# Kernel tuning notes

Hardware: AMD Instinct MI355X
Metric: run time of the kernel (lower is better)

Reference implementation:

```python
import jax, jax.numpy as jnp
import numpy as np

C, N, B = 16, 65536, 4096  # cases, points per case, batch of case IDs


def _w(key, fan_in, fan_out):
    return jax.random.normal(key, (fan_in, fan_out), dtype=jnp.float32) / np.sqrt(fan_in).astype(np.float32)


def setup_inputs() -> dict:
    key = jax.random.key(0)
    ks = jax.random.split(key, 8)
    pts = jax.random.normal(ks[0], (C, N, 3), dtype=jnp.float32)
    inp = {
        "pts": pts,
        "W1_0": _w(ks[1], 3, 64), "b1_0": jnp.zeros((64,), jnp.float32),
        "W1_1": _w(ks[2], 64, 128), "b1_1": jnp.zeros((128,), jnp.float32),
        "W1_2": _w(ks[3], 128, 512), "b1_2": jnp.zeros((512,), jnp.float32),
        "W2_0": _w(ks[4], 512, 256), "b2_0": jnp.zeros((256,), jnp.float32),
        "W2_1": _w(ks[5], 256, 512), "b2_1": jnp.zeros((512,), jnp.float32),
        "x": jax.random.randint(ks[6], (B,), 0, C, dtype=jnp.int64),
    }
    return inp


def reference(pts, W1_0, b1_0, W1_1, b1_1, W1_2, b1_2, W2_0, b2_0, W2_1, b2_1, x):
    def mlp1(h):  # shared per-point MLP, SiLU after every layer
        h = jax.nn.silu(h @ W1_0 + b1_0)
        h = jax.nn.silu(h @ W1_1 + b1_1)
        h = jax.nn.silu(h @ W1_2 + b1_2)
        return h

    feats = mlp1(pts)                       # [C, N, F1]
    idx = jnp.argmax(feats, axis=1)         # [C, F1] critical-point indices per feature
    # gather critical points (detached in the torch original)
    fixed = jax.lax.stop_gradient(pts[jnp.arange(pts.shape[0])[:, None], idx])  # [C, F1, 3]

    feats2 = mlp1(fixed)                    # [C, F1, F1]
    latent0 = jnp.max(feats2, axis=1)       # [C, F1]

    h = jax.nn.silu(latent0 @ W2_0 + b2_0)  # [C, 256]
    latent = h @ W2_1 + b2_1                # [C, total_modes*ge_features]

    caseID_unit = jax.nn.one_hot(x, latent.shape[0], dtype=latent.dtype)  # [B, C]
    return caseID_unit @ latent             # [B, 512]
```

## Files before the change

### kernel.cpp

```cpp
#include <hip/hip_runtime.h>
#include <math.h>

#define NCASES   16
#define NPTS_BIG 65536
#define F1       512
#define OUT_B    4096

typedef __attribute__((ext_vector_type(8))) short  short8;
typedef __attribute__((ext_vector_type(4))) float  floatx4;

__device__ __forceinline__ float silu_f(float x) {
    return x * __builtin_amdgcn_rcpf(1.0f + __expf(-x));
}

__device__ __forceinline__ unsigned f2bf_hi(float x) {
    unsigned u = __float_as_uint(x);
    return u + 0x7FFFu + ((u >> 16) & 1u);
}
__device__ __forceinline__ unsigned short f2bf(float x) {
    return (unsigned short)(f2bf_hi(x) >> 16);
}
__device__ __forceinline__ unsigned pk2bf_rtz(float lo, float hi) {
    return __builtin_amdgcn_perm(__float_as_uint(hi), __float_as_uint(lo), 0x07060302u);
}

__device__ __forceinline__ unsigned enc_f(float x) {
    unsigned u = __float_as_uint(x);
    return (u & 0x80000000u) ? ~u : (u | 0x80000000u);
}
__device__ __forceinline__ float dec_f(unsigned e) {
    unsigned u = (e & 0x80000000u) ? (e ^ 0x80000000u) : ~e;
    return __uint_as_float(u);
}

__device__ __forceinline__ float sgpr_f(float x) {
    return __uint_as_float(__builtin_amdgcn_readfirstlane(__float_as_uint(x)));
}

__global__ void k_prep(const float* __restrict__ W11, const float* __restrict__ W12,
                       unsigned short* __restrict__ BbWs, unsigned short* __restrict__ BcWs,
                       unsigned long long* __restrict__ argBufs)
{
    int i = blockIdx.x * 256 + threadIdx.x;
    if (i < 16384) argBufs[i] = 0ull;
    {
        int j = i & 7, l = (i >> 3) & 63, t = i >> 9;
        int KT = t & 3, NT = (t >> 2) & 3, w = t >> 4;
        int k = KT * 32 + (l >> 4) * 8 + j;
        int f = w * 64 + NT * 16 + (l & 15);
        BcWs[i] = f2bf(W12[(size_t)k * 512 + f]);
    }
    if (i < 8192) {
        int j = i & 7, l = (i >> 3) & 63, t = i >> 9;
        int KT = t & 1, w = t >> 1;
        int k = KT * 32 + (l >> 4) * 8 + j;
        int f = w * 16 + (l & 15);
        BbWs[i] = f2bf(W11[(size_t)k * 128 + f]);
    }
}

template<bool GATHER>
__global__ __launch_bounds__(512, 4)
void k_mlp1_argmax(const float* __restrict__ pts, int nPts, int chunksPerBlock,
                   const unsigned long long* __restrict__ gatherIdx,
                   const float* __restrict__ W10, const float* __restrict__ b10,
                   const float* __restrict__ b11, const float* __restrict__ b12,
                   const unsigned short* __restrict__ BbWs,
                   const unsigned short* __restrict__ BcWs,
                   unsigned long long* __restrict__ argOut)
{
    const int c   = blockIdx.y;
    const int tid = threadIdx.x;
    const int w   = tid >> 6;
    const int l   = tid & 63;
    const int lm  = l & 15;
    const int q   = l >> 4;

    __shared__ __align__(16) unsigned short s_h0[2][64][72];
    __shared__ __align__(16) unsigned short s_h1[2][64][136];

    const int wf = __builtin_amdgcn_readfirstlane(w);

    float wA0[8], wA1[8], wA2[8], bA[8];
    #pragma unroll
    for (int j = 0; j < 8; ++j) {
        wA0[j] = sgpr_f(W10[  0 + wf * 8 + j]);
        wA1[j] = sgpr_f(W10[ 64 + wf * 8 + j]);
        wA2[j] = sgpr_f(W10[128 + wf * 8 + j]);
        bA[j]  = sgpr_f(b10[       wf * 8 + j]);
    }

    short8 Bc[16];
    #pragma unroll
    for (int t = 0; t < 16; ++t)
        Bc[t] = *(const short8*)(BcWs + (size_t)((wf * 16 + t) * 64 + l) * 8);
    short8 Bb[2];
    #pragma unroll
    for (int t = 0; t < 2; ++t)
        Bb[t] = *(const short8*)(BbWs + (size_t)((wf * 2 + t) * 64 + l) * 8);

    const float bias11 = b11[wf * 16 + lm];
    const floatx4 bias4 = {bias11, bias11, bias11, bias11};
    const floatx4 zero4 = {0.f, 0.f, 0.f, 0.f};

    float bestv[4];
    #pragma unroll
    for (int NT = 0; NT < 4; ++NT) bestv[NT] = -INFINITY;

    const float* cpts = pts + (size_t)c * nPts * 3;

    auto ldpt = [&](int ch, float& x, float& y, float& z) {
        const int pbase = (blockIdx.x * chunksPerBlock + ch) * 64;
        if (GATHER) {
            unsigned gi = ~(unsigned)(gatherIdx[(size_t)c * 512 + pbase + l] & 0xFFFFFFFFull);
            const float* sp = cpts + (size_t)gi * 3;
            x = sp[0]; y = sp[1]; z = sp[2];
        } else {
            const float* sp = cpts + (size_t)(pbase + l) * 3;
            x = sp[0]; y = sp[1]; z = sp[2];
        }
    };
    auto stageA = [&](int p, float x, float y, float z) {
        float v[8];
        #pragma unroll
        for (int j = 0; j < 8; ++j) {
            float t = fmaf(z, wA2[j], bA[j]);
            t = fmaf(y, wA1[j], t);
            t = fmaf(x, wA0[j], t);
            v[j] = silu_f(t);
        }
        uint4 hv = { pk2bf_rtz(v[0], v[1]), pk2bf_rtz(v[2], v[3]),
                     pk2bf_rtz(v[4], v[5]), pk2bf_rtz(v[6], v[7]) };
        *(uint4*)&s_h0[p][l][wf * 8] = hv;
    };

    {
        float x, y, z;
        ldpt(0, x, y, z);
        stageA(0, x, y, z);
    }
    __syncthreads();

    for (int ch = 0; ch < chunksPerBlock; ++ch) {
        const int p = ch & 1;
        const bool more = (ch + 1 < chunksPerBlock);

        float nx, ny, nz;
        if (more) ldpt(ch + 1, nx, ny, nz);

        #pragma unroll
        for (int MT = 0; MT < 4; ++MT) {
            short8 a0 = *(const short8*)&s_h0[p][MT * 16 + lm][q * 8];
            short8 a1 = *(const short8*)&s_h0[p][MT * 16 + lm][32 + q * 8];
            floatx4 acc = __builtin_amdgcn_mfma_f32_16x16x32_bf16(a0, Bb[0], bias4, 0, 0, 0);
            acc = __builtin_amdgcn_mfma_f32_16x16x32_bf16(a1, Bb[1], acc, 0, 0, 0);
            #pragma unroll
            for (int r = 0; r < 4; ++r) {
                unsigned uv = __float_as_uint(silu_f(acc[r]));
                s_h1[p][MT * 16 + q * 4 + r][wf * 16 + lm] = (unsigned short)(uv >> 16);
            }
        }

        if (more) stageA(p ^ 1, nx, ny, nz);

        __syncthreads();

        const int cb0 = 127 - (ch << 4);
        #pragma unroll
        for (int MT = 0; MT < 4; ++MT) {
            short8 a[4];
            #pragma unroll
            for (int KT = 0; KT < 4; ++KT)
                a[KT] = *(const short8*)&s_h1[p][MT * 16 + lm][KT * 32 + q * 8];
            const int cbM = cb0 - (MT << 2);
            #pragma unroll
            for (int NT = 0; NT < 4; ++NT) {
                floatx4 acc = __builtin_amdgcn_mfma_f32_16x16x32_bf16(a[0], Bc[NT * 4 + 0], zero4, 0, 0, 0);
                #pragma unroll
                for (int KT = 1; KT < 4; ++KT)
                    acc = __builtin_amdgcn_mfma_f32_16x16x32_bf16(a[KT], Bc[NT * 4 + KT], acc, 0, 0, 0);
                float x0 = __uint_as_float((__float_as_uint(acc[0]) & 0xFFFFFF80u) | (unsigned)(cbM));
                float x1 = __uint_as_float((__float_as_uint(acc[1]) & 0xFFFFFF80u) | (unsigned)(cbM - 1));
                float x2 = __uint_as_float((__float_as_uint(acc[2]) & 0xFFFFFF80u) | (unsigned)(cbM - 2));
                float x3 = __uint_as_float((__float_as_uint(acc[3]) & 0xFFFFFF80u) | (unsigned)(cbM - 3));
                float t0 = fmaxf(fmaxf(x0, x1), x2);
                bestv[NT] = fmaxf(fmaxf(t0, x3), bestv[NT]);
            }
        }
    }

    #pragma unroll
    for (int NT = 0; NT < 4; ++NT) {
        unsigned u = __float_as_uint(bestv[NT]);
        int t = 127 - (int)(u & 127u);
        unsigned idx = (unsigned)((blockIdx.x * chunksPerBlock + (t >> 4)) * 64
                                  + ((t >> 2) & 3) * 16 + q * 4 + (t & 3));
        float v = __uint_as_float(u & 0xFFFFFF80u) + b12[wf * 64 + NT * 16 + lm];
        #pragma unroll
        for (int m = 16; m <= 32; m <<= 1) {
            float    vo = __shfl_xor(v, m, 64);
            unsigned io = __shfl_xor(idx, m, 64);
            if (vo > v || (vo == v && io < idx)) { v = vo; idx = io; }
        }
        if (q == 0) {
            unsigned long long key = ((unsigned long long)enc_f(v) << 32)
                                   | (unsigned long long)(~idx);
            atomicMax(&argOut[(size_t)c * 512 + wf * 64 + NT * 16 + lm], key);
        }
    }
}

__global__ __launch_bounds__(256)
void k_head(const unsigned long long* __restrict__ argBuf2,
            const float* __restrict__ W20, const float* __restrict__ b20,
            const float* __restrict__ W21, const float* __restrict__ b21,
            float* __restrict__ latent)
{
    const int c = blockIdx.x, tid = threadIdx.x;
    __shared__ float l0[512];
    __shared__ float hh[256];
    l0[tid]       = silu_f(dec_f((unsigned)(argBuf2[(size_t)c * 512 + tid] >> 32)));
    l0[tid + 256] = silu_f(dec_f((unsigned)(argBuf2[(size_t)c * 512 + tid + 256] >> 32)));
    __syncthreads();
    float acc = b20[tid];
    for (int k = 0; k < 512; ++k) acc += l0[k] * W20[(size_t)k * 256 + tid];
    hh[tid] = silu_f(acc);
    __syncthreads();
    #pragma unroll
    for (int r = 0; r < 2; ++r) {
        int f = tid + r * 256;
        float a2 = b21[f];
        for (int k = 0; k < 256; ++k) a2 += hh[k] * W21[(size_t)k * 512 + f];
        latent[(size_t)c * 512 + f] = a2;
    }
}

__global__ void k_scatter(const int* __restrict__ x,
                          const float* __restrict__ latent,
                          float* __restrict__ out)
{
    const int b = blockIdx.x, t = threadIdx.x;
    int cid = x[b];
    const float4* src = (const float4*)(latent + (size_t)cid * 512);
    float4* dst = (float4*)(out + (size_t)b * 512);
    dst[t] = src[t];
}

extern "C" void kernel_launch(void* const* d_in, const int* in_sizes, int n_in,
                              void* d_out, int out_size, void* d_ws, size_t ws_size,
                              hipStream_t stream)
{
    const float* pts = (const float*)d_in[0];
    const float* W10 = (const float*)d_in[1];
    const float* b10 = (const float*)d_in[2];
    const float* W11 = (const float*)d_in[3];
    const float* b11 = (const float*)d_in[4];
    const float* W12 = (const float*)d_in[5];
    const float* b12 = (const float*)d_in[6];
    const float* W20 = (const float*)d_in[7];
    const float* b20 = (const float*)d_in[8];
    const float* W21 = (const float*)d_in[9];
    const float* b21 = (const float*)d_in[10];
    const int*   x   = (const int*)d_in[11];
    float* out = (float*)d_out;

    char* ws = (char*)d_ws;
    unsigned long long* argBuf  = (unsigned long long*)ws;
    unsigned long long* argBuf2 = (unsigned long long*)(ws + 65536);
    float* latent               = (float*)(ws + 131072);
    unsigned short* BbWs        = (unsigned short*)(ws + 163840);
    unsigned short* BcWs        = (unsigned short*)(ws + 180224);

    k_prep<<<dim3(256), dim3(256), 0, stream>>>(W11, W12, BbWs, BcWs, argBuf);

    k_mlp1_argmax<false><<<dim3(128, NCASES), dim3(512), 0, stream>>>(
        pts, NPTS_BIG, 8, nullptr, W10, b10, b11, b12, BbWs, BcWs, argBuf);

    k_mlp1_argmax<true><<<dim3(8, NCASES), dim3(512), 0, stream>>>(
        pts, NPTS_BIG, 1, argBuf, W10, b10, b11, b12, BbWs, BcWs, argBuf2);

    k_head<<<dim3(NCASES), dim3(256), 0, stream>>>(argBuf2, W20, b20, W21, b21, latent);

    k_scatter<<<dim3(OUT_B), dim3(128), 0, stream>>>(x, latent, out);
}
```

Measured before the change: 263.1 us.

## Fuse gathered second MLP pass and head MLP into one per-case tail kernel

Replaces the gather-mode argmax kernel (8x16 blocks with 64-bit atomics into a second buffer) and the separate head kernel with a single k_tail kernel, one 512-thread block per case. Each block runs the per-point MLP over the 512 gathered critical points, tracks only the max (no index), then applies the two head layers from shared memory. This removes one launch, the second argmax buffer, its zeroing and the atomics. In exchange the gathered pass runs on only 16 blocks instead of 128, so it has less parallelism.

Result: slower. 272.3 us (+3.5%).

```diff
diff --git a/kernel.cpp b/kernel.cpp
--- a/kernel.cpp
+++ b/kernel.cpp
@@ -8,6 +8,7 @@
 
 typedef __attribute__((ext_vector_type(8))) short  short8;
 typedef __attribute__((ext_vector_type(4))) float  floatx4;
+typedef unsigned short ush;
 
 __device__ __forceinline__ float silu_f(float x) {
     return x * __builtin_amdgcn_rcpf(1.0f + __expf(-x));
@@ -17,8 +18,8 @@
     unsigned u = __float_as_uint(x);
     return u + 0x7FFFu + ((u >> 16) & 1u);
 }
-__device__ __forceinline__ unsigned short f2bf(float x) {
-    return (unsigned short)(f2bf_hi(x) >> 16);
+__device__ __forceinline__ ush f2bf(float x) {
+    return (ush)(f2bf_hi(x) >> 16);
 }
 __device__ __forceinline__ unsigned pk2bf_rtz(float lo, float hi) {
     return __builtin_amdgcn_perm(__float_as_uint(hi), __float_as_uint(lo), 0x07060302u);
@@ -28,21 +29,16 @@
     unsigned u = __float_as_uint(x);
     return (u & 0x80000000u) ? ~u : (u | 0x80000000u);
 }
-__device__ __forceinline__ float dec_f(unsigned e) {
-    unsigned u = (e & 0x80000000u) ? (e ^ 0x80000000u) : ~e;
-    return __uint_as_float(u);
-}
 
 __device__ __forceinline__ float sgpr_f(float x) {
     return __uint_as_float(__builtin_amdgcn_readfirstlane(__float_as_uint(x)));
 }
 
 __global__ void k_prep(const float* __restrict__ W11, const float* __restrict__ W12,
-                       unsigned short* __restrict__ BbWs, unsigned short* __restrict__ BcWs,
-                       unsigned long long* __restrict__ argBufs)
+                       ush* __restrict__ BbWs, ush* __restrict__ BcWs,
+                       unsigned long long* __restrict__ argBuf)
 {
     int i = blockIdx.x * 256 + threadIdx.x;
-    if (i < 16384) argBufs[i] = 0ull;
     {
         int j = i & 7, l = (i >> 3) & 63, t = i >> 9;
         int KT = t & 3, NT = (t >> 2) & 3, w = t >> 4;
@@ -51,6 +47,7 @@
         BcWs[i] = f2bf(W12[(size_t)k * 512 + f]);
     }
     if (i < 8192) {
+        argBuf[i] = 0ull;
         int j = i & 7, l = (i >> 3) & 63, t = i >> 9;
         int KT = t & 1, w = t >> 1;
         int k = KT * 32 + (l >> 4) * 8 + j;
@@ -59,14 +56,12 @@
     }
 }
 
-template<bool GATHER>
 __global__ __launch_bounds__(512, 4)
 void k_mlp1_argmax(const float* __restrict__ pts, int nPts, int chunksPerBlock,
-                   const unsigned long long* __restrict__ gatherIdx,
                    const float* __restrict__ W10, const float* __restrict__ b10,
                    const float* __restrict__ b11, const float* __restrict__ b12,
-                   const unsigned short* __restrict__ BbWs,
-                   const unsigned short* __restrict__ BcWs,
+                   const ush* __restrict__ BbWs,
+                   const ush* __restrict__ BcWs,
                    unsigned long long* __restrict__ argOut)
 {
     const int c   = blockIdx.y;
@@ -76,8 +71,8 @@
     const int lm  = l & 15;
     const int q   = l >> 4;
 
-    __shared__ __align__(16) unsigned short s_h0[2][64][72];
-    __shared__ __align__(16) unsigned short s_h1[2][64][136];
+    __shared__ __align__(16) ush s_h0[2][64][72];
+    __shared__ __align__(16) ush s_h1[2][64][136];
 
     const int wf = __builtin_amdgcn_readfirstlane(w);
 
@@ -111,14 +106,8 @@
 
     auto ldpt = [&](int ch, float& x, float& y, float& z) {
         const int pbase = (blockIdx.x * chunksPerBlock + ch) * 64;
-        if (GATHER) {
-            unsigned gi = ~(unsigned)(gatherIdx[(size_t)c * 512 + pbase + l] & 0xFFFFFFFFull);
-            const float* sp = cpts + (size_t)gi * 3;
-            x = sp[0]; y = sp[1]; z = sp[2];
-        } else {
-            const float* sp = cpts + (size_t)(pbase + l) * 3;
-            x = sp[0]; y = sp[1]; z = sp[2];
-        }
+        const float* sp = cpts + (size_t)(pbase + l) * 3;
+        x = sp[0]; y = sp[1]; z = sp[2];
     };
     auto stageA = [&](int p, float x, float y, float z) {
         float v[8];
@@ -157,7 +146,7 @@
             #pragma unroll
             for (int r = 0; r < 4; ++r) {
                 unsigned uv = __float_as_uint(silu_f(acc[r]));
-                s_h1[p][MT * 16 + q * 4 + r][wf * 16 + lm] = (unsigned short)(uv >> 16);
+                s_h1[p][MT * 16 + q * 4 + r][wf * 16 + lm] = (ush)(uv >> 16);
             }
         }
 
@@ -210,28 +199,155 @@
     }
 }
 
-__global__ __launch_bounds__(256)
-void k_head(const unsigned long long* __restrict__ argBuf2,
+__global__ __launch_bounds__(512, 4)
+void k_tail(const float* __restrict__ pts, int nPts,
+            const unsigned long long* __restrict__ argBuf,
+            const float* __restrict__ W10, const float* __restrict__ b10,
+            const float* __restrict__ b11, const float* __restrict__ b12,
+            const ush* __restrict__ BbWs,
+            const ush* __restrict__ BcWs,
             const float* __restrict__ W20, const float* __restrict__ b20,
             const float* __restrict__ W21, const float* __restrict__ b21,
             float* __restrict__ latent)
 {
-    const int c = blockIdx.x, tid = threadIdx.x;
-    __shared__ float l0[512];
-    __shared__ float hh[256];
-    l0[tid]       = silu_f(dec_f((unsigned)(argBuf2[(size_t)c * 512 + tid] >> 32)));
-    l0[tid + 256] = silu_f(dec_f((unsigned)(argBuf2[(size_t)c * 512 + tid + 256] >> 32)));
+    const int c   = blockIdx.x;
+    const int tid = threadIdx.x;
+    const int w   = tid >> 6;
+    const int l   = tid & 63;
+    const int lm  = l & 15;
+    const int q   = l >> 4;
+
+    __shared__ __align__(16) ush s_h0[2][64][72];
+    __shared__ __align__(16) ush s_h1[2][64][136];
+    __shared__ float s_l0[512];
+    __shared__ float s_hh[256];
+
+    const int wf = __builtin_amdgcn_readfirstlane(w);
+
+    float wA0[8], wA1[8], wA2[8], bA[8];
+    #pragma unroll
+    for (int j = 0; j < 8; ++j) {
+        wA0[j] = sgpr_f(W10[  0 + wf * 8 + j]);
+        wA1[j] = sgpr_f(W10[ 64 + wf * 8 + j]);
+        wA2[j] = sgpr_f(W10[128 + wf * 8 + j]);
+        bA[j]  = sgpr_f(b10[       wf * 8 + j]);
+    }
+
+    short8 Bc[16];
+    #pragma unroll
+    for (int t = 0; t < 16; ++t)
+        Bc[t] = *(const short8*)(BcWs + (size_t)((wf * 16 + t) * 64 + l) * 8);
+    short8 Bb[2];
+    #pragma unroll
+    for (int t = 0; t < 2; ++t)
+        Bb[t] = *(const short8*)(BbWs + (size_t)((wf * 2 + t) * 64 + l) * 8);
+
+    const float bias11 = b11[wf * 16 + lm];
+    const floatx4 bias4 = {bias11, bias11, bias11, bias11};
+    const floatx4 zero4 = {0.f, 0.f, 0.f, 0.f};
+
+    float bestv[4];
+    #pragma unroll
+    for (int NT = 0; NT < 4; ++NT) bestv[NT] = -INFINITY;
+
+    const float* cpts = pts + (size_t)c * nPts * 3;
+
+    auto ldpt = [&](int ch, float& x, float& y, float& z) {
+        unsigned gi = ~(unsigned)(argBuf[(size_t)c * 512 + ch * 64 + l] & 0xFFFFFFFFull);
+        const float* sp = cpts + (size_t)gi * 3;
+        x = sp[0]; y = sp[1]; z = sp[2];
+    };
+    auto stageA = [&](int p, float x, float y, float z) {
+        float v[8];
+        #pragma unroll
+        for (int j = 0; j < 8; ++j) {
+            float t = fmaf(z, wA2[j], bA[j]);
+            t = fmaf(y, wA1[j], t);
+            t = fmaf(x, wA0[j], t);
+            v[j] = silu_f(t);
+        }
+        uint4 hv = { pk2bf_rtz(v[0], v[1]), pk2bf_rtz(v[2], v[3]),
+                     pk2bf_rtz(v[4], v[5]), pk2bf_rtz(v[6], v[7]) };
+        *(uint4*)&s_h0[p][l][wf * 8] = hv;
+    };
+
+    {
+        float x, y, z;
+        ldpt(0, x, y, z);
+        stageA(0, x, y, z);
+    }
     __syncthreads();
-    float acc = b20[tid];
-    for (int k = 0; k < 512; ++k) acc += l0[k] * W20[(size_t)k * 256 + tid];
-    hh[tid] = silu_f(acc);
+
+    #pragma unroll 1
+    for (int ch = 0; ch < 8; ++ch) {
+        const int p = ch & 1;
+        const bool more = (ch + 1 < 8);
+
+        float nx, ny, nz;
+        if (more) ldpt(ch + 1, nx, ny, nz);
+
+        #pragma unroll
+        for (int MT = 0; MT < 4; ++MT) {
+            short8 a0 = *(const short8*)&s_h0[p][MT * 16 + lm][q * 8];
+            short8 a1 = *(const short8*)&s_h0[p][MT * 16 + lm][32 + q * 8];
+            floatx4 acc = __builtin_amdgcn_mfma_f32_16x16x32_bf16(a0, Bb[0], bias4, 0, 0, 0);
+            acc = __builtin_amdgcn_mfma_f32_16x16x32_bf16(a1, Bb[1], acc, 0, 0, 0);
+            #pragma unroll
+            for (int r = 0; r < 4; ++r) {
+                unsigned uv = __float_as_uint(silu_f(acc[r]));
+                s_h1[p][MT * 16 + q * 4 + r][wf * 16 + lm] = (ush)(uv >> 16);
+            }
+        }
+
+        if (more) stageA(p ^ 1, nx, ny, nz);
+
+        __syncthreads();
+
+        #pragma unroll
+        for (int MT = 0; MT < 4; ++MT) {
+            short8 a[4];
+            #pragma unroll
+            for (int KT = 0; KT < 4; ++KT)
+                a[KT] = *(const short8*)&s_h1[p][MT * 16 + lm][KT * 32 + q * 8];
+            #pragma unroll
+            for (int NT = 0; NT < 4; ++NT) {
+                floatx4 acc = __builtin_amdgcn_mfma_f32_16x16x32_bf16(a[0], Bc[NT * 4 + 0], zero4, 0, 0, 0);
+                #pragma unroll
+                for (int KT = 1; KT < 4; ++KT)
+                    acc = __builtin_amdgcn_mfma_f32_16x16x32_bf16(a[KT], Bc[NT * 4 + KT], acc, 0, 0, 0);
+                float t0 = fmaxf(fmaxf(acc[0], acc[1]), acc[2]);
+                bestv[NT] = fmaxf(fmaxf(t0, acc[3]), bestv[NT]);
+            }
+        }
+    }
+
+    #pragma unroll
+    for (int NT = 0; NT < 4; ++NT) {
+        float v = bestv[NT];
+        #pragma unroll
+        for (int m = 16; m <= 32; m <<= 1)
+            v = fmaxf(v, __shfl_xor(v, m, 64));
+        if (q == 0) {
+            unsigned u = __float_as_uint(v) & 0xFFFFFF80u;
+            s_l0[wf * 64 + NT * 16 + lm] =
+                silu_f(__uint_as_float(u) + b12[wf * 64 + NT * 16 + lm]);
+        }
+    }
     __syncthreads();
-    #pragma unroll
-    for (int r = 0; r < 2; ++r) {
-        int f = tid + r * 256;
-        float a2 = b21[f];
-        for (int k = 0; k < 256; ++k) a2 += hh[k] * W21[(size_t)k * 512 + f];
-        latent[(size_t)c * 512 + f] = a2;
+
+    if (tid < 256) {
+        float acc = b20[tid];
+        for (int k = 0; k < 512; ++k)
+            acc = fmaf(s_l0[k], W20[(size_t)k * 256 + tid], acc);
+        s_hh[tid] = silu_f(acc);
+    }
+    __syncthreads();
+
+    {
+        float a2 = b21[tid];
+        for (int k = 0; k < 256; ++k)
+            a2 = fmaf(s_hh[k], W21[(size_t)k * 512 + tid], a2);
+        latent[(size_t)c * 512 + tid] = a2;
     }
 }
 
@@ -266,20 +382,18 @@
 
     char* ws = (char*)d_ws;
     unsigned long long* argBuf  = (unsigned long long*)ws;
-    unsigned long long* argBuf2 = (unsigned long long*)(ws + 65536);
-    float* latent               = (float*)(ws + 131072);
-    unsigned short* BbWs        = (unsigned short*)(ws + 163840);
-    unsigned short* BcWs        = (unsigned short*)(ws + 180224);
+    float* latent               = (float*)(ws + 65536);
+    ush* BbWs                   = (ush*)(ws + 98304);
+    ush* BcWs                   = (ush*)(ws + 114688);
 
     k_prep<<<dim3(256), dim3(256), 0, stream>>>(W11, W12, BbWs, BcWs, argBuf);
 
-    k_mlp1_argmax<false><<<dim3(128, NCASES), dim3(512), 0, stream>>>(
-        pts, NPTS_BIG, 8, nullptr, W10, b10, b11, b12, BbWs, BcWs, argBuf);
-
-    k_mlp1_argmax<true><<<dim3(8, NCASES), dim3(512), 0, stream>>>(
-        pts, NPTS_BIG, 1, argBuf, W10, b10, b11, b12, BbWs, BcWs, argBuf2);
-
-    k_head<<<dim3(NCASES), dim3(256), 0, stream>>>(argBuf2, W20, b20, W21, b21, latent);
+    k_mlp1_argmax<<<dim3(128, NCASES), dim3(512), 0, stream>>>(
+        pts, NPTS_BIG, 8, W10, b10, b11, b12, BbWs, BcWs, argBuf);
+
+    k_tail<<<dim3(NCASES), dim3(512), 0, stream>>>(
+        pts, NPTS_BIG, argBuf, W10, b10, b11, b12, BbWs, BcWs,
+        W20, b20, W21, b21, latent);
 
     k_scatter<<<dim3(OUT_B), dim3(128), 0, stream>>>(x, latent, out);
 }
```

## Fuse head MLP and case scatter into gather kernel via last-block counter

Applied to the files above, without the earlier changes.

Removes the separate head and scatter kernels by having the last block per case (detected with an atomic done counter after a threadfence) compute the two-layer head and write output rows for matching batch IDs. The counters are zeroed in the prep kernel by extending its clear range. This saves two kernel launches and the latent round-trip through memory. The cost is that the head runs on only 16 blocks, and each block scans the full ID list and writes up to hundreds of rows serially, which may be slower than the wide scatter grid.

Result: slower. 313.6 us (+19.2%).

```diff
diff --git a/kernel.cpp b/kernel.cpp
--- a/kernel.cpp
+++ b/kernel.cpp
@@ -8,6 +8,7 @@
 
 typedef __attribute__((ext_vector_type(8))) short  short8;
 typedef __attribute__((ext_vector_type(4))) float  floatx4;
+typedef unsigned short ush;
 
 __device__ __forceinline__ float silu_f(float x) {
     return x * __builtin_amdgcn_rcpf(1.0f + __expf(-x));
@@ -17,8 +18,8 @@
     unsigned u = __float_as_uint(x);
     return u + 0x7FFFu + ((u >> 16) & 1u);
 }
-__device__ __forceinline__ unsigned short f2bf(float x) {
-    return (unsigned short)(f2bf_hi(x) >> 16);
+__device__ __forceinline__ ush f2bf(float x) {
+    return (ush)(f2bf_hi(x) >> 16);
 }
 __device__ __forceinline__ unsigned pk2bf_rtz(float lo, float hi) {
     return __builtin_amdgcn_perm(__float_as_uint(hi), __float_as_uint(lo), 0x07060302u);
@@ -38,11 +39,11 @@
 }
 
 __global__ void k_prep(const float* __restrict__ W11, const float* __restrict__ W12,
-                       unsigned short* __restrict__ BbWs, unsigned short* __restrict__ BcWs,
+                       ush* __restrict__ BbWs, ush* __restrict__ BcWs,
                        unsigned long long* __restrict__ argBufs)
 {
     int i = blockIdx.x * 256 + threadIdx.x;
-    if (i < 16384) argBufs[i] = 0ull;
+    if (i < 16400) argBufs[i] = 0ull;
     {
         int j = i & 7, l = (i >> 3) & 63, t = i >> 9;
         int KT = t & 3, NT = (t >> 2) & 3, w = t >> 4;
@@ -65,9 +66,13 @@
                    const unsigned long long* __restrict__ gatherIdx,
                    const float* __restrict__ W10, const float* __restrict__ b10,
                    const float* __restrict__ b11, const float* __restrict__ b12,
-                   const unsigned short* __restrict__ BbWs,
-                   const unsigned short* __restrict__ BcWs,
-                   unsigned long long* __restrict__ argOut)
+                   const ush* __restrict__ BbWs,
+                   const ush* __restrict__ BcWs,
+                   unsigned long long* __restrict__ argOut,
+                   const float* __restrict__ W20, const float* __restrict__ b20,
+                   const float* __restrict__ W21, const float* __restrict__ b21,
+                   const int* __restrict__ x, float* __restrict__ out,
+                   unsigned long long* __restrict__ doneCnt)
 {
     const int c   = blockIdx.y;
     const int tid = threadIdx.x;
@@ -76,8 +81,8 @@
     const int lm  = l & 15;
     const int q   = l >> 4;
 
-    __shared__ __align__(16) unsigned short s_h0[2][64][72];
-    __shared__ __align__(16) unsigned short s_h1[2][64][136];
+    __shared__ __align__(16) ush s_h0[2][64][72];
+    __shared__ __align__(16) ush s_h1[2][64][136];
 
     const int wf = __builtin_amdgcn_readfirstlane(w);
 
@@ -109,24 +114,24 @@
 
     const float* cpts = pts + (size_t)c * nPts * 3;
 
-    auto ldpt = [&](int ch, float& x, float& y, float& z) {
+    auto ldpt = [&](int ch, float& xx, float& yy, float& zz) {
         const int pbase = (blockIdx.x * chunksPerBlock + ch) * 64;
         if (GATHER) {
             unsigned gi = ~(unsigned)(gatherIdx[(size_t)c * 512 + pbase + l] & 0xFFFFFFFFull);
             const float* sp = cpts + (size_t)gi * 3;
-            x = sp[0]; y = sp[1]; z = sp[2];
+            xx = sp[0]; yy = sp[1]; zz = sp[2];
         } else {
             const float* sp = cpts + (size_t)(pbase + l) * 3;
-            x = sp[0]; y = sp[1]; z = sp[2];
+            xx = sp[0]; yy = sp[1]; zz = sp[2];
         }
     };
-    auto stageA = [&](int p, float x, float y, float z) {
+    auto stageA = [&](int p, float xx, float yy, float zz) {
         float v[8];
         #pragma unroll
         for (int j = 0; j < 8; ++j) {
-            float t = fmaf(z, wA2[j], bA[j]);
-            t = fmaf(y, wA1[j], t);
-            t = fmaf(x, wA0[j], t);
+            float t = fmaf(zz, wA2[j], bA[j]);
+            t = fmaf(yy, wA1[j], t);
+            t = fmaf(xx, wA0[j], t);
             v[j] = silu_f(t);
         }
         uint4 hv = { pk2bf_rtz(v[0], v[1]), pk2bf_rtz(v[2], v[3]),
@@ -135,9 +140,9 @@
     };
 
     {
-        float x, y, z;
-        ldpt(0, x, y, z);
-        stageA(0, x, y, z);
+        float xx, yy, zz;
+        ldpt(0, xx, yy, zz);
+        stageA(0, xx, yy, zz);
     }
     __syncthreads();
 
@@ -157,7 +162,7 @@
             #pragma unroll
             for (int r = 0; r < 4; ++r) {
                 unsigned uv = __float_as_uint(silu_f(acc[r]));
-                s_h1[p][MT * 16 + q * 4 + r][wf * 16 + lm] = (unsigned short)(uv >> 16);
+                s_h1[p][MT * 16 + q * 4 + r][wf * 16 + lm] = (ush)(uv >> 16);
             }
         }
 
@@ -208,42 +213,53 @@
             atomicMax(&argOut[(size_t)c * 512 + wf * 64 + NT * 16 + lm], key);
         }
     }
-}
-
-__global__ __launch_bounds__(256)
-void k_head(const unsigned long long* __restrict__ argBuf2,
-            const float* __restrict__ W20, const float* __restrict__ b20,
-            const float* __restrict__ W21, const float* __restrict__ b21,
-            float* __restrict__ latent)
-{
-    const int c = blockIdx.x, tid = threadIdx.x;
-    __shared__ float l0[512];
-    __shared__ float hh[256];
-    l0[tid]       = silu_f(dec_f((unsigned)(argBuf2[(size_t)c * 512 + tid] >> 32)));
-    l0[tid + 256] = silu_f(dec_f((unsigned)(argBuf2[(size_t)c * 512 + tid + 256] >> 32)));
-    __syncthreads();
-    float acc = b20[tid];
-    for (int k = 0; k < 512; ++k) acc += l0[k] * W20[(size_t)k * 256 + tid];
-    hh[tid] = silu_f(acc);
-    __syncthreads();
-    #pragma unroll
-    for (int r = 0; r < 2; ++r) {
-        int f = tid + r * 256;
-        float a2 = b21[f];
-        for (int k = 0; k < 256; ++k) a2 += hh[k] * W21[(size_t)k * 512 + f];
-        latent[(size_t)c * 512 + f] = a2;
-    }
-}
-
-__global__ void k_scatter(const int* __restrict__ x,
-                          const float* __restrict__ latent,
-                          float* __restrict__ out)
-{
-    const int b = blockIdx.x, t = threadIdx.x;
-    int cid = x[b];
-    const float4* src = (const float4*)(latent + (size_t)cid * 512);
-    float4* dst = (float4*)(out + (size_t)b * 512);
-    dst[t] = src[t];
+
+    if constexpr (GATHER) {
+        __threadfence();
+        __syncthreads();
+        __shared__ unsigned long long s_old;
+        if (tid == 0) s_old = atomicAdd(&doneCnt[c], 1ull);
+        __syncthreads();
+        if (s_old == 7ull) {
+            __threadfence();
+            __shared__ float s_l0[512];
+            __shared__ float s_part[2][256];
+            __shared__ float s_hh[256];
+            __shared__ int   s_list[4096];
+            __shared__ int   s_n;
+            unsigned long long key = atomicMax(&argOut[(size_t)c * 512 + tid], 0ull);
+            s_l0[tid] = silu_f(dec_f((unsigned)(key >> 32)));
+            if (tid == 0) s_n = 0;
+            __syncthreads();
+            {
+                const int h = tid & 255, half = tid >> 8;
+                const float* wcol = W20 + (size_t)(half * 256) * 256 + h;
+                const float* lv   = s_l0 + half * 256;
+                float acc = 0.f;
+                #pragma unroll 4
+                for (int k = 0; k < 256; ++k)
+                    acc = fmaf(lv[k], wcol[(size_t)k * 256], acc);
+                s_part[half][h] = acc;
+            }
+            __syncthreads();
+            if (tid < 256)
+                s_hh[tid] = silu_f(s_part[0][tid] + s_part[1][tid] + b20[tid]);
+            __syncthreads();
+            float lat = b21[tid];
+            #pragma unroll 4
+            for (int k = 0; k < 256; ++k)
+                lat = fmaf(s_hh[k], W21[(size_t)k * 512 + tid], lat);
+            #pragma unroll
+            for (int r = 0; r < 8; ++r) {
+                int b = r * 512 + tid;
+                if (x[b] == c) { int pos = atomicAdd(&s_n, 1); s_list[pos] = b; }
+            }
+            __syncthreads();
+            const int n = s_n;
+            for (int i = 0; i < n; ++i)
+                out[(size_t)s_list[i] * 512 + tid] = lat;
+        }
+    }
 }
 
 extern "C" void kernel_launch(void* const* d_in, const int* in_sizes, int n_in,
@@ -267,19 +283,17 @@
     char* ws = (char*)d_ws;
     unsigned long long* argBuf  = (unsigned long long*)ws;
     unsigned long long* argBuf2 = (unsigned long long*)(ws + 65536);
-    float* latent               = (float*)(ws + 131072);
-    unsigned short* BbWs        = (unsigned short*)(ws + 163840);
-    unsigned short* BcWs        = (unsigned short*)(ws + 180224);
+    unsigned long long* doneCnt = (unsigned long long*)(ws + 131072);
+    ush* BbWs                   = (ush*)(ws + 131200);
+    ush* BcWs                   = (ush*)(ws + 147584);
 
     k_prep<<<dim3(256), dim3(256), 0, stream>>>(W11, W12, BbWs, BcWs, argBuf);
 
     k_mlp1_argmax<false><<<dim3(128, NCASES), dim3(512), 0, stream>>>(
-        pts, NPTS_BIG, 8, nullptr, W10, b10, b11, b12, BbWs, BcWs, argBuf);
+        pts, NPTS_BIG, 8, nullptr, W10, b10, b11, b12, BbWs, BcWs, argBuf,
+        nullptr, nullptr, nullptr, nullptr, nullptr, nullptr, nullptr);
 
     k_mlp1_argmax<true><<<dim3(8, NCASES), dim3(512), 0, stream>>>(
-        pts, NPTS_BIG, 1, argBuf, W10, b10, b11, b12, BbWs, BcWs, argBuf2);
-
-    k_head<<<dim3(NCASES), dim3(256), 0, stream>>>(argBuf2, W20, b20, W21, b21, latent);
-
-    k_scatter<<<dim3(OUT_B), dim3(128), 0, stream>>>(x, latent, out);
-}
+        pts, NPTS_BIG, 1, argBuf, W10, b10, b11, b12, BbWs, BcWs, argBuf2,
+        W20, b20, W21, b21, x, out, doneCnt);
+}
```
